# Kernel optimization log

Measured on AMD Instinct MI355X. Metric: run time of the kernel, lower is better.

Reference implementation:

```python
import jax, jax.numpy as jnp
import numpy as np
import math

D_MODEL = 1024
N_HEADS = 16
D_HEAD = D_MODEL // N_HEADS


def setup_inputs() -> dict:
    key = jax.random.key(0)
    k_x, k_wqkv, k_bqkv, k_wp, k_bp = jax.random.split(key, 5)
    B, T = 2, 2048
    s = 1.0 / math.sqrt(D_MODEL)
    return {
        "x": jax.random.normal(k_x, (B, T, D_MODEL), dtype=jnp.float32),
        "W_qkv": jax.random.uniform(k_wqkv, (D_MODEL, 3 * D_MODEL), minval=-s, maxval=s, dtype=jnp.float32),
        "b_qkv": jax.random.uniform(k_bqkv, (3 * D_MODEL,), minval=-s, maxval=s, dtype=jnp.float32),
        "W_proj": jax.random.uniform(k_wp, (D_MODEL, D_MODEL), minval=-s, maxval=s, dtype=jnp.float32),
        "b_proj": jax.random.uniform(k_bp, (D_MODEL,), minval=-s, maxval=s, dtype=jnp.float32),
    }


def reference(x, W_qkv, b_qkv, W_proj, b_proj):
    B, T, C = x.shape
    qkv = x @ W_qkv + b_qkv                      # [B,T,3C]
    qkv = qkv.reshape(B, T, 3, N_HEADS, D_HEAD)
    qkv = jnp.transpose(qkv, (2, 0, 3, 1, 4))     # [3,B,H,T,dh]
    q, k, v = qkv[0], qkv[1], qkv[2]
    scale = math.sqrt(D_HEAD)
    attn = jnp.einsum('bhqd,bhkd->bhqk', q, k) / scale  # [B,H,T,T]
    causal = jnp.tril(jnp.ones((T, T), dtype=bool))
    attn = jnp.where(causal, attn, -jnp.inf)
    attn = jax.nn.softmax(attn, axis=-1)
    out = jnp.einsum('bhqk,bhkd->bhqd', attn, v)  # [B,H,T,dh]
    out = jnp.transpose(out, (0, 2, 1, 3)).reshape(B, T, C)
    return out @ W_proj + b_proj
```

## Files before the change

kernel.cpp:

```cpp
#include <hip/hip_runtime.h>

#define B_    2
#define T_    2048
#define C_    1024
#define H_    16
#define DH_   64
#define M_    (B_ * T_)
#define NQKV  (3 * C_)

typedef __bf16 bf16;
typedef __bf16 bf16x4 __attribute__((ext_vector_type(4)));
typedef __bf16 bf16x8 __attribute__((ext_vector_type(8)));
typedef float  f32x4  __attribute__((ext_vector_type(4)));

__device__ __forceinline__ void async16(const void* g, void* l) {
  __builtin_amdgcn_global_load_lds(
      (const __attribute__((address_space(1))) void*)g,
      (__attribute__((address_space(3))) void*)l, 16, 0, 0);
}

__global__ __launch_bounds__(256) void cvt_bf16_k(const float* __restrict__ in,
                                                  bf16* __restrict__ out) {
  const int i = (blockIdx.x * 256 + threadIdx.x) * 4;
  float4 v = *(const float4*)(in + i);
  bf16x4 o;
  o[0] = (bf16)v.x; o[1] = (bf16)v.y; o[2] = (bf16)v.z; o[3] = (bf16)v.w;
  *(bf16x4*)(out + i) = o;
}

__global__ __launch_bounds__(256) void transpose_cvt(const float* __restrict__ in,
                                                     bf16* __restrict__ out,
                                                     int R, int C) {
  __shared__ float tile[32][33];
  const int c0 = blockIdx.x * 32, r0 = blockIdx.y * 32;
  const int tx = threadIdx.x, ty = threadIdx.y;
#pragma unroll
  for (int j = 0; j < 4; j++)
    tile[ty + j * 8][tx] = in[(size_t)(r0 + ty + j * 8) * C + c0 + tx];
  __syncthreads();
#pragma unroll
  for (int j = 0; j < 4; j++)
    out[(size_t)(c0 + ty + j * 8) * R + r0 + tx] = (bf16)tile[tx][ty + j * 8];
}

template <int EPI>
__global__ __launch_bounds__(256) void gemm128(
    const bf16* __restrict__ A, const bf16* __restrict__ Bt,
    const float* __restrict__ bias, float* __restrict__ outF,
    bf16* __restrict__ qb, bf16* __restrict__ kb, bf16* __restrict__ vtb) {
  constexpr int K = 1024;
  __shared__ alignas(16) bf16 As[128 * 32];
  __shared__ alignas(16) bf16 Bs[128 * 32];
  const int tid = threadIdx.x;
  const int lane = tid & 63, wv = tid >> 6;
  const int l15 = lane & 15, quad = lane >> 4;
  const int wm = (wv >> 1) * 64, wn = (wv & 1) * 64;
  const int m0 = blockIdx.x * 128, n0 = blockIdx.y * 128;

  f32x4 acc[4][4] = {};

  const int arow = tid >> 2;
  const int ag = (tid & 3) ^ ((arow >> 1) & 3);
  const bf16* ga = A + (size_t)(m0 + arow) * K + ag * 8;
  const bf16* gb = Bt + (size_t)(n0 + arow) * K + ag * 8;
  bf16* lA = As + tid * 8;
  bf16* lB = Bs + tid * 8;
  const int rg = (quad ^ ((l15 >> 1) & 3)) * 8;

  for (int k0 = 0; k0 < K; k0 += 32) {
    async16(ga + k0, lA);
    async16(ga + k0 + (size_t)64 * K, lA + 2048);
    async16(gb + k0, lB);
    async16(gb + k0 + (size_t)64 * K, lB + 2048);
    __syncthreads();
    bf16x8 af[4], bfr[4];
#pragma unroll
    for (int i = 0; i < 4; i++)
      af[i] = *(const bf16x8*)(As + (wm + i * 16 + l15) * 32 + rg);
#pragma unroll
    for (int j = 0; j < 4; j++)
      bfr[j] = *(const bf16x8*)(Bs + (wn + j * 16 + l15) * 32 + rg);
#pragma unroll
    for (int i = 0; i < 4; i++)
#pragma unroll
      for (int j = 0; j < 4; j++)
        acc[i][j] = __builtin_amdgcn_mfma_f32_16x16x32_bf16(af[i], bfr[j],
                                                            acc[i][j], 0, 0, 0);
    __syncthreads();
  }

#pragma unroll
  for (int i = 0; i < 4; i++) {
#pragma unroll
    for (int j = 0; j < 4; j++) {
      const int gcol = n0 + wn + j * 16 + l15;
      const float bv = bias[gcol];
#pragma unroll
      for (int r = 0; r < 4; r++) {
        const int grow = m0 + wm + i * 16 + quad * 4 + r;
        float v = acc[i][j][r] + bv;
        if constexpr (EPI == 0) {
          const int which = gcol >> 10;
          const int hn = gcol & 1023;
          const int h = hn >> 6, d = hn & 63;
          const int bb = grow >> 11, t = grow & 2047;
          const int head = bb * 16 + h;
          if (which == 0)
            qb[head * 131072 + t * 64 + d] = (bf16)(v * 0.1803368801f);
          else if (which == 1)
            kb[head * 131072 + t * 64 + d] = (bf16)v;
          else
            vtb[head * 131072 + d * 2048 + t] = (bf16)v;
        } else {
          outF[(size_t)grow * 1024 + gcol] = v;
        }
      }
    }
  }
}

__global__ __launch_bounds__(512) void attn_k(const bf16* __restrict__ Q,
                                              const bf16* __restrict__ K,
                                              const bf16* __restrict__ Vt,
                                              bf16* __restrict__ O) {
  __shared__ alignas(16) bf16 Ks[2][64 * 64];
  __shared__ alignas(16) bf16 Vs[2][64 * 64];
  __shared__ alignas(16) bf16 Ps[8][16 * 64];
  const int tid = threadIdx.x, lane = tid & 63, wv = tid >> 6;
  const int l15 = lane & 15, quad = lane >> 4;

  const int b = blockIdx.x;
  const int bh = (b & 7) | ((b >> 6) << 3);
  const int xpair = (b >> 3) & 7;

  const bf16* Qb = Q + (size_t)bh * 131072;
  const bf16* Kb = K + (size_t)bh * 131072;
  const bf16* Vb = Vt + (size_t)bh * 131072;

  const int srow = tid >> 3;
  const int sg = (tid & 7) ^ (srow & 7);
  const bf16* gk = Kb + srow * 64 + sg * 8;
  const bf16* gv = Vb + srow * 2048 + sg * 8;
  const int swz = l15 & 7;
  bf16* Pw = Ps[wv];
  const int bb = bh >> 4, h = bh & 15;

  for (int t = 0; t < 2; ++t) {
    const int qJ = t ? (15 - xpair) : xpair;
    const int q0 = qJ * 128;
    const int nIter = 2 * qJ + 2;
    const int q = q0 + wv * 16 + l15;

    bf16x8 aq0 = *(const bf16x8*)(Qb + q * 64 + quad * 8);
    bf16x8 aq1 = *(const bf16x8*)(Qb + q * 64 + 32 + quad * 8);

    f32x4 o[4] = {};
    float m = -3.0e38f, lsum = 0.f;

    async16(gk, &Ks[0][tid * 8]);
    async16(gv, &Vs[0][tid * 8]);

    for (int it = 0; it < nIter; ++it) {
      __syncthreads();
      const bf16* Kc = Ks[it & 1];
      const bf16* Vc = Vs[it & 1];

      bf16x8 kf[2][4];
#pragma unroll
      for (int kc = 0; kc < 2; kc++)
#pragma unroll
        for (int nf = 0; nf < 4; nf++)
          kf[kc][nf] = *(const bf16x8*)(Kc + (nf * 16 + l15) * 64 +
                                        (((kc * 4 + quad) ^ swz) * 8));

      if (it + 1 < nIter) {
        const int kt1 = (it + 1) * 64;
        const int nb = (it + 1) & 1;
        async16(gk + kt1 * 64, &Ks[nb][tid * 8]);
        async16(gv + kt1, &Vs[nb][tid * 8]);
      }

      f32x4 s[4] = {};
#pragma unroll
      for (int kc = 0; kc < 2; kc++) {
        bf16x8 a = kc ? aq1 : aq0;
#pragma unroll
        for (int nf = 0; nf < 4; nf++)
          s[nf] = __builtin_amdgcn_mfma_f32_16x16x32_bf16(kf[kc][nf], a, s[nf], 0, 0, 0);
      }

      if (it >= nIter - 2) {
#pragma unroll
        for (int nf = 0; nf < 4; nf++)
#pragma unroll
          for (int r = 0; r < 4; r++) {
            const int kt = it * 64 + nf * 16 + quad * 4 + r;
            if (kt > q) s[nf][r] = -3.0e38f;
          }
      }

      float mx = s[0][0];
#pragma unroll
      for (int nf = 0; nf < 4; nf++)
#pragma unroll
        for (int r = 0; r < 4; r++) mx = fmaxf(mx, s[nf][r]);
      mx = fmaxf(mx, __shfl_xor(mx, 16));
      mx = fmaxf(mx, __shfl_xor(mx, 32));
      const float mnew = fmaxf(m, mx);
      const float alpha = __builtin_amdgcn_exp2f(m - mnew);
      m = mnew;
      float ts = 0.f;
      bf16x4 p4[4];
#pragma unroll
      for (int nf = 0; nf < 4; nf++)
#pragma unroll
        for (int r = 0; r < 4; r++) {
          const float pv = __builtin_amdgcn_exp2f(s[nf][r] - mnew);
          ts += pv;
          p4[nf][r] = (bf16)pv;
        }
      ts += __shfl_xor(ts, 16);
      ts += __shfl_xor(ts, 32);
      lsum = lsum * alpha + ts;
#pragma unroll
      for (int nf = 0; nf < 4; nf++)
#pragma unroll
        for (int r = 0; r < 4; r++) o[nf][r] *= alpha;

#pragma unroll
      for (int nf = 0; nf < 4; nf++)
        *(bf16x4*)(Pw + l15 * 64 + ((((nf << 1) | (quad >> 1)) ^ swz) << 3) +
                   ((quad & 1) << 2)) = p4[nf];

      bf16x8 pb0 = *(const bf16x8*)(Pw + l15 * 64 + ((quad ^ swz) << 3));
      bf16x8 pb1 = *(const bf16x8*)(Pw + l15 * 64 + (((4 + quad) ^ swz) << 3));

#pragma unroll
      for (int kc = 0; kc < 2; kc++) {
        bf16x8 pb = kc ? pb1 : pb0;
#pragma unroll
        for (int nf = 0; nf < 4; nf++) {
          bf16x8 vf = *(const bf16x8*)(Vc + (nf * 16 + l15) * 64 +
                                       (((kc * 4 + quad) ^ swz) * 8));
          o[nf] = __builtin_amdgcn_mfma_f32_16x16x32_bf16(vf, pb, o[nf], 0, 0, 0);
        }
      }
    }

    const float inv = 1.0f / lsum;
#pragma unroll
    for (int nf = 0; nf < 4; nf++) {
      bf16x4 ov;
#pragma unroll
      for (int r = 0; r < 4; r++) ov[r] = (bf16)(o[nf][r] * inv);
      *(bf16x4*)(O + (size_t)(bb * 2048 + q) * 1024 + h * 64 + nf * 16 + quad * 4) = ov;
    }
  }
}

extern "C" void kernel_launch(void* const* d_in, const int* in_sizes, int n_in,
                              void* d_out, int out_size, void* d_ws, size_t ws_size,
                              hipStream_t stream) {
  const float* x     = (const float*)d_in[0];
  const float* Wqkv  = (const float*)d_in[1];
  const float* bqkv  = (const float*)d_in[2];
  const float* Wproj = (const float*)d_in[3];
  const float* bproj = (const float*)d_in[4];
  float* out = (float*)d_out;

  char* p = (char*)d_ws;
  bf16* xbf    = (bf16*)p; p += (size_t)M_ * C_ * 2;
  bf16* wqkvT  = (bf16*)p; p += (size_t)NQKV * C_ * 2;
  bf16* wprojT = (bf16*)p; p += (size_t)C_ * C_ * 2;
  bf16* Qb     = (bf16*)p; p += (size_t)M_ * C_ * 2;
  bf16* Kb     = (bf16*)p; p += (size_t)M_ * C_ * 2;
  bf16* Vtb    = (bf16*)p; p += (size_t)M_ * C_ * 2;
  bf16* AO     = (bf16*)p;

  cvt_bf16_k<<<M_ * C_ / 1024, 256, 0, stream>>>(x, xbf);
  transpose_cvt<<<dim3(NQKV / 32, C_ / 32), dim3(32, 8), 0, stream>>>(Wqkv, wqkvT, C_, NQKV);
  transpose_cvt<<<dim3(C_ / 32, C_ / 32), dim3(32, 8), 0, stream>>>(Wproj, wprojT, C_, C_);

  gemm128<0><<<dim3(M_ / 128, NQKV / 128), 256, 0, stream>>>(
      xbf, wqkvT, bqkv, nullptr, Qb, Kb, Vtb);

  attn_k<<<256, 512, 0, stream>>>(Qb, Kb, Vtb, AO);

  gemm128<1><<<dim3(M_ / 128, C_ / 128), 256, 0, stream>>>(
      AO, wprojT, bproj, out, nullptr, nullptr, nullptr);
}
```

Before: 184.2 us.

## Double attention KV tile to 128 keys per iteration with wider LDS swizzle

The flash-attention kernel now processes 128 keys per iteration instead of 64. This halves the number of barriers, online-softmax rescales and loop iterations per query tile, and causal masking is applied only on the final iteration. LDS use per block doubles to about 96KB, and launch bounds ask for 2 blocks per CU, which adds register pressure from twice as many score fragments. The V and P layouts switch to a 16-way XOR swizzle to match the 128-wide rows.

```diff
diff --git a/kernel.cpp b/kernel.cpp
--- a/kernel.cpp
+++ b/kernel.cpp
@@ -119,13 +119,13 @@
   }
 }
 
-__global__ __launch_bounds__(512) void attn_k(const bf16* __restrict__ Q,
-                                              const bf16* __restrict__ K,
-                                              const bf16* __restrict__ Vt,
-                                              bf16* __restrict__ O) {
-  __shared__ alignas(16) bf16 Ks[2][64 * 64];
-  __shared__ alignas(16) bf16 Vs[2][64 * 64];
-  __shared__ alignas(16) bf16 Ps[8][16 * 64];
+__global__ __launch_bounds__(512, 2) void attn_k(const bf16* __restrict__ Q,
+                                                 const bf16* __restrict__ K,
+                                                 const bf16* __restrict__ Vt,
+                                                 bf16* __restrict__ O) {
+  __shared__ alignas(16) bf16 Ks[2][128 * 64];
+  __shared__ alignas(16) bf16 Vs[2][64 * 128];
+  __shared__ alignas(16) bf16 Ps[8][16 * 128];
   const int tid = threadIdx.x, lane = tid & 63, wv = tid >> 6;
   const int l15 = lane & 15, quad = lane >> 4;
 
@@ -137,18 +137,21 @@
   const bf16* Kb = K + (size_t)bh * 131072;
   const bf16* Vb = Vt + (size_t)bh * 131072;
 
-  const int srow = tid >> 3;
-  const int sg = (tid & 7) ^ (srow & 7);
-  const bf16* gk = Kb + srow * 64 + sg * 8;
-  const bf16* gv = Vb + srow * 2048 + sg * 8;
-  const int swz = l15 & 7;
+  const int krow = tid >> 3;
+  const int kg = (tid & 7) ^ (krow & 7);
+  const bf16* gk = Kb + krow * 64 + kg * 8;
+  const int vrow = tid >> 4;
+  const int vg = (tid & 15) ^ (vrow & 15);
+  const bf16* gv = Vb + vrow * 2048 + vg * 8;
+
+  const int swz7 = l15 & 7;
   bf16* Pw = Ps[wv];
   const int bb = bh >> 4, h = bh & 15;
 
   for (int t = 0; t < 2; ++t) {
     const int qJ = t ? (15 - xpair) : xpair;
     const int q0 = qJ * 128;
-    const int nIter = 2 * qJ + 2;
+    const int nIter = qJ + 1;
     const int q = q0 + wv * 16 + l15;
 
     bf16x8 aq0 = *(const bf16x8*)(Qb + q * 64 + quad * 8);
@@ -157,51 +160,56 @@
     f32x4 o[4] = {};
     float m = -3.0e38f, lsum = 0.f;
 
+    __syncthreads();
     async16(gk, &Ks[0][tid * 8]);
+    async16(gk + 64 * 64, &Ks[0][tid * 8 + 4096]);
     async16(gv, &Vs[0][tid * 8]);
+    async16(gv + 32 * 2048, &Vs[0][tid * 8 + 4096]);
 
     for (int it = 0; it < nIter; ++it) {
       __syncthreads();
       const bf16* Kc = Ks[it & 1];
       const bf16* Vc = Vs[it & 1];
 
-      bf16x8 kf[2][4];
+      bf16x8 kf[2][8];
 #pragma unroll
       for (int kc = 0; kc < 2; kc++)
 #pragma unroll
-        for (int nf = 0; nf < 4; nf++)
+        for (int nf = 0; nf < 8; nf++)
           kf[kc][nf] = *(const bf16x8*)(Kc + (nf * 16 + l15) * 64 +
-                                        (((kc * 4 + quad) ^ swz) * 8));
+                                        (((kc * 4 + quad) ^ swz7) << 3));
 
       if (it + 1 < nIter) {
-        const int kt1 = (it + 1) * 64;
+        const int kt1 = (it + 1) * 128;
         const int nb = (it + 1) & 1;
         async16(gk + kt1 * 64, &Ks[nb][tid * 8]);
+        async16(gk + kt1 * 64 + 64 * 64, &Ks[nb][tid * 8 + 4096]);
         async16(gv + kt1, &Vs[nb][tid * 8]);
-      }
-
-      f32x4 s[4] = {};
+        async16(gv + kt1 + 32 * 2048, &Vs[nb][tid * 8 + 4096]);
+      }
+
+      f32x4 s[8] = {};
 #pragma unroll
       for (int kc = 0; kc < 2; kc++) {
         bf16x8 a = kc ? aq1 : aq0;
 #pragma unroll
-        for (int nf = 0; nf < 4; nf++)
+        for (int nf = 0; nf < 8; nf++)
           s[nf] = __builtin_amdgcn_mfma_f32_16x16x32_bf16(kf[kc][nf], a, s[nf], 0, 0, 0);
       }
 
-      if (it >= nIter - 2) {
-#pragma unroll
-        for (int nf = 0; nf < 4; nf++)
+      if (it == nIter - 1) {
+#pragma unroll
+        for (int nf = 0; nf < 8; nf++)
 #pragma unroll
           for (int r = 0; r < 4; r++) {
-            const int kt = it * 64 + nf * 16 + quad * 4 + r;
+            const int kt = it * 128 + nf * 16 + quad * 4 + r;
             if (kt > q) s[nf][r] = -3.0e38f;
           }
       }
 
       float mx = s[0][0];
 #pragma unroll
-      for (int nf = 0; nf < 4; nf++)
+      for (int nf = 0; nf < 8; nf++)
 #pragma unroll
         for (int r = 0; r < 4; r++) mx = fmaxf(mx, s[nf][r]);
       mx = fmaxf(mx, __shfl_xor(mx, 16));
@@ -210,9 +218,9 @@
       const float alpha = __builtin_amdgcn_exp2f(m - mnew);
       m = mnew;
       float ts = 0.f;
-      bf16x4 p4[4];
-#pragma unroll
-      for (int nf = 0; nf < 4; nf++)
+      bf16x4 p4[8];
+#pragma unroll
+      for (int nf = 0; nf < 8; nf++)
 #pragma unroll
         for (int r = 0; r < 4; r++) {
           const float pv = __builtin_amdgcn_exp2f(s[nf][r] - mnew);
@@ -228,23 +236,23 @@
         for (int r = 0; r < 4; r++) o[nf][r] *= alpha;
 
 #pragma unroll
-      for (int nf = 0; nf < 4; nf++)
-        *(bf16x4*)(Pw + l15 * 64 + ((((nf << 1) | (quad >> 1)) ^ swz) << 3) +
+      for (int nf = 0; nf < 8; nf++)
+        *(bf16x4*)(Pw + l15 * 128 + ((((nf << 1) | (quad >> 1)) ^ l15) << 3) +
                    ((quad & 1) << 2)) = p4[nf];
 
-      bf16x8 pb0 = *(const bf16x8*)(Pw + l15 * 64 + ((quad ^ swz) << 3));
-      bf16x8 pb1 = *(const bf16x8*)(Pw + l15 * 64 + (((4 + quad) ^ swz) << 3));
-
-#pragma unroll
-      for (int kc = 0; kc < 2; kc++) {
-        bf16x8 pb = kc ? pb1 : pb0;
+      bf16x8 pb[4];
+#pragma unroll
+      for (int kc = 0; kc < 4; kc++)
+        pb[kc] = *(const bf16x8*)(Pw + l15 * 128 + (((kc * 4 + quad) ^ l15) << 3));
+
+#pragma unroll
+      for (int kc = 0; kc < 4; kc++)
 #pragma unroll
         for (int nf = 0; nf < 4; nf++) {
-          bf16x8 vf = *(const bf16x8*)(Vc + (nf * 16 + l15) * 64 +
-                                       (((kc * 4 + quad) ^ swz) * 8));
-          o[nf] = __builtin_amdgcn_mfma_f32_16x16x32_bf16(vf, pb, o[nf], 0, 0, 0);
+          bf16x8 vf = *(const bf16x8*)(Vc + (nf * 16 + l15) * 128 +
+                                       (((kc * 4 + quad) ^ l15) << 3));
+          o[nf] = __builtin_amdgcn_mfma_f32_16x16x32_bf16(vf, pb[kc], o[nf], 0, 0, 0);
         }
-      }
     }
 
     const float inv = 1.0f / lsum;
```

Measured after the change: 177.5 us. -3.6%, faster.
